# Kernel tuning notes

Hardware: AMD Instinct MI355X
Metric: run time of the kernel (lower is better)

Reference implementation:

```python
import jax, jax.numpy as jnp
import numpy as np
import math

B, NX, NY = 4, 64, 64
IN_DIM, OUT_DIM = 3, 3
DIM, DEPTH, HEADS, DH, FF_MULT = 192, 6, 8, 64, 4
INNER = HEADS * DH              # 512
FF = DIM * FF_MULT              # 768
M = int(DH * math.log(DH))      # 266 random features (performer default)
GROUPS = 8
LATENT_STEPS = 1
EPS_SN, EPS_K, EPS_GN = 1e-5, 1e-4, 1e-5


def setup_inputs() -> dict:
    rng = np.random.default_rng(0)
    f = lambda *s: jnp.asarray(rng.standard_normal(s).astype(np.float32) * 0.02)
    # unitary forward operator (SVD-whitened in torch == orthogonal matrix)
    Q, _ = np.linalg.qr(rng.standard_normal((DIM, DIM)).astype(np.float32))
    return {
        "x": jnp.asarray(rng.standard_normal((B, NX, NY, IN_DIM)).astype(np.float32)),
        "to_in_w": f(DIM, IN_DIM), "to_in_b": f(DIM),
        "pos_emb": f(1, NX * NY, DIM),
        "proj": jnp.asarray(rng.standard_normal((DEPTH, M, DH)).astype(np.float32)),
        "sn_attn_g": jnp.ones((DEPTH,), jnp.float32),
        "wq": f(DEPTH, INNER, DIM), "wk": f(DEPTH, INNER, DIM), "wv": f(DEPTH, INNER, DIM),
        "wo": f(DEPTH, DIM, INNER), "bo": f(DEPTH, DIM),
        "sn_ff_g": jnp.ones((DEPTH,), jnp.float32),
        "w1": f(DEPTH, FF, DIM), "b1": f(DEPTH, FF),
        "w2": f(DEPTH, DIM, FF), "b2": f(DEPTH, DIM),
        "expand_w": f(DIM, DIM),
        "fwd_w": jnp.asarray(Q.astype(np.float32)),
        "dec_lin_w": f(DIM, DIM), "dec_lin_b": f(DIM),
        "gn_g": jnp.ones((DIM,), jnp.float32), "gn_b": jnp.zeros((DIM,), jnp.float32),
        "c9_w": f(DIM, DIM // GROUPS, 9, 9), "c9_b": f(DIM),
        "c7_w": f(DIM // 2, DIM // GROUPS, 7, 7), "c7_b": f(DIM // 2),
        "c5_w": f(DIM // 4, (DIM // 2) // GROUPS, 5, 5), "c5_b": f(DIM // 4),
        "c1_w": f(OUT_DIM, DIM // 4, 1, 1), "c1_b": f(OUT_DIM),
        "latent_steps": LATENT_STEPS,
    }


def _scalenorm(x, g):
    n = jnp.linalg.norm(x, axis=-1, keepdims=True) * (x.shape[-1] ** -0.5)
    return x / jnp.maximum(n, EPS_SN) * g


def _softmax_features(data, proj, is_query):
    # data: [b,h,n,d]; proj: [m,d] -> FAVOR+ softmax-kernel features [b,h,n,m]
    dn = data.shape[-1] ** -0.25
    ratio = proj.shape[0] ** -0.5
    dd = jnp.einsum('bhnd,md->bhnm', data * dn, proj)
    diag = 0.5 * jnp.sum(data * data, -1) * (dn * dn)  # [b,h,n]
    if is_query:
        mx = jnp.max(dd, axis=-1, keepdims=True)
    else:
        mx = jnp.max(dd, axis=(-1, -2), keepdims=True)
    return ratio * (jnp.exp(dd - diag[..., None] - mx) + EPS_K)


def _attn(x, proj, wq, wk, wv, wo, bo):
    b, n, _ = x.shape
    split = lambda t: t.reshape(b, n, HEADS, DH).transpose(0, 2, 1, 3)
    q = split(x @ wq.T); k = split(x @ wk.T); v = split(x @ wv.T)
    qp = _softmax_features(q, proj, True)
    kp = _softmax_features(k, proj, False)
    context = jnp.einsum('bhnm,bhnd->bhmd', kp, v)            # [b,h,m,d]
    denom = jnp.einsum('bhnm,bhm->bhn', qp, kp.sum(2))
    out = jnp.einsum('bhnm,bhmd->bhnd', qp, context) / denom[..., None]
    out = out.transpose(0, 2, 1, 3).reshape(b, n, INNER)
    return out @ wo.T + bo


def _circ_conv(x, w, b, groups):
    p = w.shape[-1] // 2
    x = jnp.pad(x, ((0, 0), (0, 0), (p, p), (p, p)), mode='wrap')
    y = jax.lax.conv_general_dilated(x, w, (1, 1), 'VALID',
        dimension_numbers=('NCHW', 'OIHW', 'NCHW'), feature_group_count=groups)
    return y + b[None, :, None, None]


def _group_norm(x, g, b):
    B_, C, H, W = x.shape
    xg = x.reshape(B_, GROUPS, C // GROUPS, H, W)
    mu = xg.mean((2, 3, 4), keepdims=True)
    var = xg.var((2, 3, 4), keepdims=True)
    xn = ((xg - mu) * jax.lax.rsqrt(var + EPS_GN)).reshape(B_, C, H, W)
    return xn * g[None, :, None, None] + b[None, :, None, None]


def reference(x, to_in_w, to_in_b, pos_emb, proj, sn_attn_g, wq, wk, wv, wo, bo,
              sn_ff_g, w1, b1, w2, b2, expand_w, fwd_w, dec_lin_w, dec_lin_b,
              gn_g, gn_b, c9_w, c9_b, c7_w, c7_b, c5_w, c5_b, c1_w, c1_b, latent_steps):
    b, nx, ny, _ = x.shape
    h = x @ to_in_w.T + to_in_b                       # [b,nx,ny,dim]
    h = h.reshape(b, nx * ny, DIM) + pos_emb[:, :nx * ny]
    for i in range(DEPTH):                             # Performer: prenorm attn + prenorm FF
        h = h + _attn(_scalenorm(h, sn_attn_g[i]), proj[i], wq[i], wk[i], wv[i], wo[i], bo[i])
        hn = _scalenorm(h, sn_ff_g[i])
        h = h + (jax.nn.gelu(hn @ w1[i].T + b1[i], approximate=False) @ w2[i].T + b2[i])
    h = h.reshape(b, nx, ny, DIM) @ expand_w.T        # expand_latent (no bias)
    u, us = h, []
    for _ in range(latent_steps):
        u = u @ fwd_w.T                               # unitary forward operator
        us.append(u)
    u = jnp.concatenate(us, 0)                        # [(b*t), nx, ny, c]
    y = u @ dec_lin_w.T + dec_lin_b
    y = y.transpose(0, 3, 1, 2)                       # NCHW
    y = _group_norm(y, gn_g, gn_b)
    y = jax.nn.gelu(_circ_conv(y, c9_w, c9_b, GROUPS), approximate=False)
    y = jax.nn.gelu(_circ_conv(y, c7_w, c7_b, GROUPS), approximate=False)
    y = jax.nn.gelu(_circ_conv(y, c5_w, c5_b, GROUPS), approximate=False)
    y = jax.lax.conv_general_dilated(y, c1_w, (1, 1), 'VALID',
        dimension_numbers=('NCHW', 'OIHW', 'NCHW')) + c1_b[None, :, None, None]
    # einops '(b t) c nx ny -> b t nx ny c'
    y = y.reshape(b, latent_steps, OUT_DIM, nx, ny).transpose(0, 1, 3, 4, 2)
    return y
```

## Files before the change

kernel.cpp:

```cpp
#include <hip/hip_runtime.h>
#include <cmath>

#define NB      4
#define NTOK    4096
#define BNTOK   16384
#define CDIM    192
#define CINNER  512
#define NHEADS  8
#define DHEAD   64
#define CFF     768
#define MFEAT   266
#define NDEPTH  6

#define DN      0.35355339059327373f
#define RATIO   0.06131393394849658f

typedef unsigned short u16;
typedef __attribute__((ext_vector_type(8))) short s16x8;
typedef __attribute__((ext_vector_type(8))) u16  u16x8;
typedef __attribute__((ext_vector_type(4))) float f32x4;

#define OFF_H    0ull
#define OFF_HN   3145728ull
#define OFF_Q    6291456ull
#define OFF_K    14680064ull
#define OFF_V    23068672ull
#define OFF_BIG  31457280ull
#define OFF_PJ   44040192ull
#define OFF_CTXT 44163072ull
#define OFF_KMAX 47368192ull
#define OFF_GNP  47368448ull
#define OFF_GNS  47369472ull
#define OFF_WHI  47370240ull
#define OFF_WLO  49489920ull
#define WOFF_QKV 0ull
#define WOFF_WO  1769472ull
#define WOFF_W1  2359296ull
#define WOFF_W2  3244032ull
#define WOFF_EXP 4128768ull
#define WOFF_FWD 4165632ull
#define WOFF_DEC 4202496ull

#define PJL      20480
#define CTXTN    819200

__device__ __forceinline__ float gelu_f(float x) {
    return 0.5f * x * (1.0f + erff(x * 0.7071067811865476f));
}
__device__ __forceinline__ unsigned f2ord(float f) {
    int i = __float_as_int(f);
    return (i >= 0) ? ((unsigned)i | 0x80000000u) : (unsigned)(~i);
}
__device__ __forceinline__ float ord2f(unsigned u) {
    int i = (u & 0x80000000u) ? (int)(u & 0x7fffffffu) : ~(int)u;
    return __int_as_float(i);
}
__device__ __forceinline__ void split_bf16(float a, u16& h, u16& l) {
    unsigned ua = __float_as_uint(a);
    unsigned rh = (ua + 0x7FFFu + ((ua >> 16) & 1u)) >> 16;
    h = (u16)rh;
    float hf = __uint_as_float(rh << 16);
    float lo = a - hf;
    unsigned ul = __float_as_uint(lo);
    unsigned rl = (ul + 0x7FFFu + ((ul >> 16) & 1u)) >> 16;
    l = (u16)rl;
}
__device__ __forceinline__ u16 hi_bf16(float a) {
    unsigned ua = __float_as_uint(a);
    return (u16)((ua + 0x7FFFu + ((ua >> 16) & 1u)) >> 16);
}

__global__ __launch_bounds__(256) void cvt_qkv(const float* __restrict__ wq,
    const float* __restrict__ wk, const float* __restrict__ wv,
    u16* __restrict__ hi, u16* __restrict__ lo)
{
    int idx = blockIdx.x * 256 + threadIdx.x;
    int l = idx / 294912, rem = idx - l * 294912;
    int r = rem / 192, c = rem - r * 192;
    float v;
    if (r < 512)       v = wq[((size_t)l * 512 + r) * 192 + c];
    else if (r < 1024) v = wk[((size_t)l * 512 + (r - 512)) * 192 + c];
    else               v = wv[((size_t)l * 512 + (r - 1024)) * 192 + c];
    u16 h, lw; split_bf16(v, h, lw);
    hi[idx] = h; lo[idx] = lw;
}

__global__ __launch_bounds__(256) void cvt_w(const float* __restrict__ src,
    u16* __restrict__ hi, u16* __restrict__ lo, int n)
{
    int idx = blockIdx.x * 256 + threadIdx.x;
    if (idx < n) {
        u16 h, l; split_bf16(src[idx], h, l);
        hi[idx] = h; lo[idx] = l;
    }
}

__global__ __launch_bounds__(256) void cvt_dec(const float* __restrict__ e,
    const float* __restrict__ f, const float* __restrict__ d,
    u16* __restrict__ hi, u16* __restrict__ lo)
{
    int idx = blockIdx.x * 256 + threadIdx.x;
    if (idx >= 110592) return;
    int which = idx / 36864, rem = idx - which * 36864;
    float v = (which == 0) ? e[rem] : (which == 1) ? f[rem] : d[rem];
    u16 h, l; split_bf16(v, h, l);
    hi[idx] = h; lo[idx] = l;
}

__global__ __launch_bounds__(256) void cvt_pj(const float* __restrict__ proj,
    u16* __restrict__ hi, u16* __restrict__ lo)
{
    int idx = blockIdx.x * 256 + threadIdx.x;
    int l = idx / PJL, rem = idx - l * PJL;
    int m = rem >> 6, k = rem & 63;
    float v = (m < MFEAT) ? proj[(size_t)l * MFEAT * DHEAD + m * 64 + k] : 0.f;
    u16 h, lw; split_bf16(v, h, lw);
    hi[idx] = h; lo[idx] = lw;
}

__global__ __launch_bounds__(256) void input_embed(const float* __restrict__ x,
    const float* __restrict__ w, const float* __restrict__ bvec,
    const float* __restrict__ pos, float* __restrict__ h)
{
    int idx = blockIdx.x * 256 + threadIdx.x;
    int row = idx / CDIM, c = idx - row * CDIM;
    int p = row & (NTOK - 1);
    const float* xr = x + (size_t)row * 3;
    h[idx] = xr[0]*w[c*3+0] + xr[1]*w[c*3+1] + xr[2]*w[c*3+2] + bvec[c] + pos[(size_t)p*CDIM + c];
}

__global__ __launch_bounds__(256) void scalenorm_kernel(const float* __restrict__ in,
    float* __restrict__ out, const float* __restrict__ gptr, int gidx)
{
    int wv = threadIdx.x >> 6, lane = threadIdx.x & 63;
    int row = blockIdx.x * 4 + wv;
    const float* p = in + (size_t)row * CDIM;
    float x0 = p[lane], x1 = p[lane + 64], x2 = p[lane + 128];
    float ss = x0*x0 + x1*x1 + x2*x2;
    #pragma unroll
    for (int off = 32; off; off >>= 1) ss += __shfl_xor(ss, off);
    float g = gptr[gidx];
    float n = sqrtf(ss * (1.0f / 192.0f));
    float s = g / fmaxf(n, 1e-5f);
    float* o = out + (size_t)row * CDIM;
    o[lane] = x0 * s; o[lane + 64] = x1 * s; o[lane + 128] = x2 * s;
}

#define LP 40
__global__ __launch_bounds__(256) void gemm_mfma(const float* __restrict__ A,
    const u16* __restrict__ Bhi, const u16* __restrict__ Blo,
    const float* __restrict__ bias, const float* __restrict__ resid,
    float* __restrict__ C, int M, int N, int K, int epi)
{
    __shared__ u16 a_hi[128 * LP], a_lo[128 * LP], b_hi[128 * LP], b_lo[128 * LP];
    const int tid = threadIdx.x;
    const int n0 = blockIdx.x * 128, m0 = blockIdx.y * 128;
    const int wave = tid >> 6, lane = tid & 63;
    const int wr = wave >> 1, wc = wave & 1;
    const int fr = lane & 15, q = lane >> 4;
    const bool wactive = (n0 + wc * 64) < N;
    f32x4 acc[4][4];
    #pragma unroll
    for (int i = 0; i < 4; ++i)
        #pragma unroll
        for (int j = 0; j < 4; ++j) { acc[i][j][0]=0.f; acc[i][j][1]=0.f; acc[i][j][2]=0.f; acc[i][j][3]=0.f; }

    const int srow = tid >> 1, sc0 = (tid & 1) * 16;
    const float* aptr = A + (size_t)(m0 + srow) * K + sc0;
    const bool bval = (n0 + srow) < N;
    const u16* bhp = Bhi + (size_t)(n0 + srow) * K + sc0;
    const u16* blp = Blo + (size_t)(n0 + srow) * K + sc0;
    const int soff = srow * LP + sc0;
    const int aoffb = (wr * 64 + fr) * LP + q * 8;
    const int boffb = (wc * 64 + fr) * LP + q * 8;

    for (int kc = 0; kc < K; kc += 32) {
        float4 f0 = *(const float4*)(aptr + kc);
        float4 f1 = *(const float4*)(aptr + kc + 4);
        float4 f2 = *(const float4*)(aptr + kc + 8);
        float4 f3 = *(const float4*)(aptr + kc + 12);
        u16x8 h0, l0, h1, l1;
        {
            float v[16] = {f0.x,f0.y,f0.z,f0.w, f1.x,f1.y,f1.z,f1.w,
                           f2.x,f2.y,f2.z,f2.w, f3.x,f3.y,f3.z,f3.w};
            u16 hh[16], ll[16];
            #pragma unroll
            for (int i = 0; i < 16; ++i) split_bf16(v[i], hh[i], ll[i]);
            #pragma unroll
            for (int i = 0; i < 8; ++i) { h0[i]=hh[i]; l0[i]=ll[i]; h1[i]=hh[8+i]; l1[i]=ll[8+i]; }
        }
        *(u16x8*)&a_hi[soff]     = h0;  *(u16x8*)&a_hi[soff + 8] = h1;
        *(u16x8*)&a_lo[soff]     = l0;  *(u16x8*)&a_lo[soff + 8] = l1;
        u16x8 bh0 = (u16x8)0, bh1 = (u16x8)0, bl0 = (u16x8)0, bl1 = (u16x8)0;
        if (bval) {
            bh0 = *(const u16x8*)(bhp + kc);  bh1 = *(const u16x8*)(bhp + kc + 8);
            bl0 = *(const u16x8*)(blp + kc);  bl1 = *(const u16x8*)(blp + kc + 8);
        }
        *(u16x8*)&b_hi[soff]     = bh0;  *(u16x8*)&b_hi[soff + 8] = bh1;
        *(u16x8*)&b_lo[soff]     = bl0;  *(u16x8*)&b_lo[soff + 8] = bl1;
        __syncthreads();
        if (wactive) {
            s16x8 Ah[4], Al[4], Bh[4], Bl[4];
            #pragma unroll
            for (int t = 0; t < 4; ++t) {
                Ah[t] = *(const s16x8*)&a_hi[aoffb + t * 16 * LP];
                Al[t] = *(const s16x8*)&a_lo[aoffb + t * 16 * LP];
                Bh[t] = *(const s16x8*)&b_hi[boffb + t * 16 * LP];
                Bl[t] = *(const s16x8*)&b_lo[boffb + t * 16 * LP];
            }
            #pragma unroll
            for (int i = 0; i < 4; ++i)
                #pragma unroll
                for (int j = 0; j < 4; ++j)
                    acc[i][j] = __builtin_amdgcn_mfma_f32_16x16x32_bf16(Ah[i], Bh[j], acc[i][j], 0, 0, 0);
            #pragma unroll
            for (int i = 0; i < 4; ++i)
                #pragma unroll
                for (int j = 0; j < 4; ++j)
                    acc[i][j] = __builtin_amdgcn_mfma_f32_16x16x32_bf16(Ah[i], Bl[j], acc[i][j], 0, 0, 0);
            #pragma unroll
            for (int i = 0; i < 4; ++i)
                #pragma unroll
                for (int j = 0; j < 4; ++j)
                    acc[i][j] = __builtin_amdgcn_mfma_f32_16x16x32_bf16(Al[i], Bh[j], acc[i][j], 0, 0, 0);
        }
        __syncthreads();
    }
    const int c0 = n0 + wc * 64;
    const int rowb = m0 + wr * 64;
    #pragma unroll
    for (int j = 0; j < 4; ++j) {
        int c = c0 + j * 16 + fr;
        if (c >= N) continue;
        float bb = (epi & 1) ? bias[c] : 0.f;
        float* cp;
        if (epi & 8) cp = C + (size_t)(c >> 9) * 8388608ull + (size_t)(c & 511);
        else         cp = C + c;
        const float* rp = (epi & 4) ? (resid + c) : nullptr;
        #pragma unroll
        for (int i = 0; i < 4; ++i) {
            #pragma unroll
            for (int r = 0; r < 4; ++r) {
                int row = rowb + i * 16 + q * 4 + r;
                float val = acc[i][j][r] + bb;
                if (epi & 2) val = gelu_f(val);
                if (epi & 4) val += rp[(size_t)row * N];
                size_t off = (epi & 8) ? (size_t)row * 512 : (size_t)row * N;
                cp[off] = val;
            }
        }
    }
}

__global__ void kmax_init(unsigned* kmaxu) {
    if (threadIdx.x < NDEPTH * 32) kmaxu[threadIdx.x] = 0u;
}

__global__ __launch_bounds__(256) void kmax2_kernel(const float* __restrict__ Km,
    const u16* __restrict__ pjh, unsigned* __restrict__ kmaxu)
{
    __shared__ __align__(16) u16 khi[64 * 72];
    __shared__ float wred[4];
    const int tid = threadIdx.x;
    const int nt = blockIdx.x, bh = blockIdx.y;
    const int b = bh >> 3, hh = bh & 7;
    const int wave = tid >> 6, lane = tid & 63;
    const int fr = lane & 15, quad = lane >> 4;
    float lm = -1e30f;
    const size_t kbase = ((size_t)b * NTOK) * CINNER + hh * DHEAD;
    for (int ch = 0; ch < 4; ++ch) {
        const int n0 = nt * 256 + ch * 64;
        __syncthreads();
        {
            int tok = tid >> 2, koff = (tid & 3) * 16;
            const float* kp = Km + kbase + (size_t)(n0 + tok) * CINNER + koff;
            u16 hh16[16];
            #pragma unroll
            for (int qd = 0; qd < 4; ++qd) {
                float4 f = *(const float4*)(kp + qd * 4);
                hh16[qd*4+0] = hi_bf16(f.x * DN); hh16[qd*4+1] = hi_bf16(f.y * DN);
                hh16[qd*4+2] = hi_bf16(f.z * DN); hh16[qd*4+3] = hi_bf16(f.w * DN);
            }
            u16x8 v0, v1;
            #pragma unroll
            for (int i = 0; i < 8; ++i) { v0[i] = hh16[i]; v1[i] = hh16[8+i]; }
            *(u16x8*)&khi[tok * 72 + koff] = v0;
            *(u16x8*)&khi[tok * 72 + koff + 8] = v1;
        }
        __syncthreads();
        int rowA = (wave * 16 + fr) * 72;
        s16x8 A0 = *(const s16x8*)&khi[rowA + quad * 8];
        s16x8 A1 = *(const s16x8*)&khi[rowA + 32 + quad * 8];
        for (int ct = 0; ct < 17; ++ct) {
            const u16* bp = pjh + (ct * 16 + fr) * 64 + quad * 8;
            s16x8 B0 = *(const s16x8*)bp;
            s16x8 B1 = *(const s16x8*)(bp + 32);
            f32x4 t; t[0]=0.f; t[1]=0.f; t[2]=0.f; t[3]=0.f;
            t = __builtin_amdgcn_mfma_f32_16x16x32_bf16(A0, B0, t, 0, 0, 0);
            t = __builtin_amdgcn_mfma_f32_16x16x32_bf16(A1, B1, t, 0, 0, 0);
            if (ct * 16 + fr < MFEAT) {
                #pragma unroll
                for (int r = 0; r < 4; ++r) lm = fmaxf(lm, t[r]);
            }
        }
    }
    #pragma unroll
    for (int off = 32; off; off >>= 1) lm = fmaxf(lm, __shfl_xor(lm, off));
    if (lane == 0) wred[wave] = lm;
    __syncthreads();
    if (tid == 0) {
        float m = fmaxf(fmaxf(wred[0], wred[1]), fmaxf(wred[2], wred[3]));
        atomicMax(kmaxu + bh, f2ord(m));
    }
}

__global__ __launch_bounds__(256) void ctx2_kernel(const float* __restrict__ Km,
    const float* __restrict__ Vm, const u16* __restrict__ pjh, const u16* __restrict__ pjl,
    const unsigned* __restrict__ kmaxu, float* __restrict__ part)
{
    __shared__ __align__(16) u16 khi[32 * 72], klo[32 * 72];
    __shared__ __align__(16) u16 vth[80 * 40], vtl[80 * 40];
    __shared__ __align__(16) u16 kph[4][16 * 40], kpl[4][16 * 40];
    __shared__ float diag[32];
    const int tid = threadIdx.x;
    const int bh = blockIdx.x, seg = blockIdx.y;
    const int b = bh >> 3, hh = bh & 7;
    const int wave = tid >> 6, lane = tid & 63;
    const int fr = lane & 15, quad = lane >> 4;
    const float kmx = ord2f(kmaxu[bh]);
    for (int i = tid; i < 16 * 40; i += 256) {
        int row = 64 + i / 40, col = i - (i / 40) * 40;
        vth[row * 40 + col] = (row == 64) ? (u16)0x3F80 : (u16)0;
        vtl[row * 40 + col] = 0;
    }
    f32x4 accv[5][5];
    #pragma unroll
    for (int i = 0; i < 5; ++i)
        #pragma unroll
        for (int j = 0; j < 5; ++j) { accv[i][j][0]=0.f; accv[i][j][1]=0.f; accv[i][j][2]=0.f; accv[i][j][3]=0.f; }
    const size_t rowbase = ((size_t)b * NTOK) * CINNER + hh * DHEAD;
    u16* sh = kph[wave];  u16* sl = kpl[wave];
    for (int nc = 0; nc < 16; ++nc) {
        const int n0 = seg * 512 + nc * 32;
        __syncthreads();
        {
            int tok = tid >> 3, koff = (tid & 7) * 8;
            const float* kp = Km + rowbase + (size_t)(n0 + tok) * CINNER + koff;
            float4 f0 = *(const float4*)kp;
            float4 f1 = *(const float4*)(kp + 4);
            float v[8] = {f0.x*DN, f0.y*DN, f0.z*DN, f0.w*DN, f1.x*DN, f1.y*DN, f1.z*DN, f1.w*DN};
            u16x8 hv, lv; float ps = 0.f;
            #pragma unroll
            for (int i = 0; i < 8; ++i) { u16 h, l; split_bf16(v[i], h, l); hv[i]=h; lv[i]=l; ps += v[i]*v[i]; }
            *(u16x8*)&khi[tok * 72 + koff] = hv;
            *(u16x8*)&klo[tok * 72 + koff] = lv;
            ps += __shfl_xor(ps, 1); ps += __shfl_xor(ps, 2); ps += __shfl_xor(ps, 4);
            if ((tid & 7) == 0) diag[tok] = 0.5f * ps;
            const float* vp = Vm + rowbase + (size_t)(n0 + tok) * CINNER + koff;
            float4 g0 = *(const float4*)vp;
            float4 g1 = *(const float4*)(vp + 4);
            float vv[8] = {g0.x, g0.y, g0.z, g0.w, g1.x, g1.y, g1.z, g1.w};
            #pragma unroll
            for (int i = 0; i < 8; ++i) {
                u16 h, l; split_bf16(vv[i], h, l);
                vth[(koff + i) * 40 + tok] = h;
                vtl[(koff + i) * 40 + tok] = l;
            }
        }
        __syncthreads();
        s16x8 Ah[2][2], Al[2][2];
        #pragma unroll
        for (int rt = 0; rt < 2; ++rt) {
            int rowA = (rt * 16 + fr) * 72;
            Ah[rt][0] = *(const s16x8*)&khi[rowA + quad * 8];
            Ah[rt][1] = *(const s16x8*)&khi[rowA + 32 + quad * 8];
            Al[rt][0] = *(const s16x8*)&klo[rowA + quad * 8];
            Al[rt][1] = *(const s16x8*)&klo[rowA + 32 + quad * 8];
        }
        for (int mc = 0; mc < 5; ++mc) {
            const int ct = mc * 4 + wave;
            const u16* bph = pjh + (ct * 16 + fr) * 64 + quad * 8;
            const u16* bpl = pjl + (ct * 16 + fr) * 64 + quad * 8;
            s16x8 B0h = *(const s16x8*)bph, B1h = *(const s16x8*)(bph + 32);
            s16x8 B0l = *(const s16x8*)bpl, B1l = *(const s16x8*)(bpl + 32);
            const bool valid = (ct * 16 + fr) < MFEAT;
            #pragma unroll
            for (int rt = 0; rt < 2; ++rt) {
                f32x4 dd; dd[0]=0.f; dd[1]=0.f; dd[2]=0.f; dd[3]=0.f;
                dd = __builtin_amdgcn_mfma_f32_16x16x32_bf16(Ah[rt][0], B0h, dd, 0, 0, 0);
                dd = __builtin_amdgcn_mfma_f32_16x16x32_bf16(Ah[rt][0], B0l, dd, 0, 0, 0);
                dd = __builtin_amdgcn_mfma_f32_16x16x32_bf16(Al[rt][0], B0h, dd, 0, 0, 0);
                dd = __builtin_amdgcn_mfma_f32_16x16x32_bf16(Ah[rt][1], B1h, dd, 0, 0, 0);
                dd = __builtin_amdgcn_mfma_f32_16x16x32_bf16(Ah[rt][1], B1l, dd, 0, 0, 0);
                dd = __builtin_amdgcn_mfma_f32_16x16x32_bf16(Al[rt][1], B1h, dd, 0, 0, 0);
                ushort4 ph, pl;
                #pragma unroll
                for (int r = 0; r < 4; ++r) {
                    float dgv = diag[rt * 16 + quad * 4 + r];
                    float val = valid ? RATIO * (expf(dd[r] - dgv - kmx) + 1e-4f) : 0.f;
                    u16 h, l; split_bf16(val, h, l);
                    (&ph.x)[r] = h; (&pl.x)[r] = l;
                }
                *(ushort4*)&sh[fr * 40 + rt * 16 + quad * 4] = ph;
                *(ushort4*)&sl[fr * 40 + rt * 16 + quad * 4] = pl;
            }
            s16x8 Bh = *(const s16x8*)&sh[fr * 40 + quad * 8];
            s16x8 Bl = *(const s16x8*)&sl[fr * 40 + quad * 8];
            #pragma unroll
            for (int rt2 = 0; rt2 < 5; ++rt2) {
                s16x8 Vh = *(const s16x8*)&vth[(rt2 * 16 + fr) * 40 + quad * 8];
                s16x8 Vl = *(const s16x8*)&vtl[(rt2 * 16 + fr) * 40 + quad * 8];
                accv[rt2][mc] = __builtin_amdgcn_mfma_f32_16x16x32_bf16(Vh, Bh, accv[rt2][mc], 0, 0, 0);
                accv[rt2][mc] = __builtin_amdgcn_mfma_f32_16x16x32_bf16(Vh, Bl, accv[rt2][mc], 0, 0, 0);
                accv[rt2][mc] = __builtin_amdgcn_mfma_f32_16x16x32_bf16(Vl, Bh, accv[rt2][mc], 0, 0, 0);
            }
        }
    }
    float* pb = part + ((size_t)(seg * 32 + bh)) * 80 * 320;
    #pragma unroll
    for (int rt2 = 0; rt2 < 5; ++rt2) {
        #pragma unroll
        for (int mc = 0; mc < 5; ++mc) {
            int ct = mc * 4 + wave;
            #pragma unroll
            for (int r = 0; r < 4; ++r)
                pb[(size_t)(rt2 * 16 + quad * 4 + r) * 320 + ct * 16 + fr] = accv[rt2][mc][r];
        }
    }
}

__global__ __launch_bounds__(256) void ctxt_reduce(const float* __restrict__ part,
    u16* __restrict__ cth, u16* __restrict__ ctl)
{
    int idx = blockIdx.x * 256 + threadIdx.x;
    float s = 0.f;
    #pragma unroll
    for (int sg = 0; sg < 8; ++sg) s += part[(size_t)sg * CTXTN + idx];
    u16 h, l; split_bf16(s, h, l);
    cth[idx] = h; ctl[idx] = l;
}

__global__ __launch_bounds__(256) void qside2_kernel(const float* __restrict__ Qm,
    const u16* __restrict__ pjh, const u16* __restrict__ pjl,
    const u16* __restrict__ cth, const u16* __restrict__ ctl,
    float* __restrict__ attn_out)
{
    __shared__ __align__(16) u16 qhi[64 * 72], qlo[64 * 72];
    __shared__ __align__(16) u16 slabh[4][16 * 72], slabl[4][16 * 72];
    __shared__ float diag[64];
    const int tid = threadIdx.x;
    const int nt = blockIdx.x, bh = blockIdx.y;
    const int b = bh >> 3, hh = bh & 7;
    const int wave = tid >> 6, lane = tid & 63;
    const int fr = lane & 15, quad = lane >> 4;
    const int n0 = nt * 64;
    {
        int tok = tid >> 2, koff = (tid & 3) * 16;
        const float* qp = Qm + ((size_t)(b * NTOK + n0 + tok)) * CINNER + hh * DHEAD + koff;
        float v[16]; float ps = 0.f;
        #pragma unroll
        for (int qd = 0; qd < 4; ++qd) {
            float4 f = *(const float4*)(qp + qd * 4);
            v[qd*4+0]=f.x*DN; v[qd*4+1]=f.y*DN; v[qd*4+2]=f.z*DN; v[qd*4+3]=f.w*DN;
        }
        u16x8 h0, l0, h1, l1;
        #pragma unroll
        for (int i = 0; i < 8; ++i) {
            u16 h, l; split_bf16(v[i], h, l); h0[i]=h; l0[i]=l;
            split_bf16(v[8+i], h, l); h1[i]=h; l1[i]=l;
        }
        #pragma unroll
        for (int i = 0; i < 16; ++i) ps += v[i]*v[i];
        *(u16x8*)&qhi[tok * 72 + koff] = h0;  *(u16x8*)&qhi[tok * 72 + koff + 8] = h1;
        *(u16x8*)&qlo[tok * 72 + koff] = l0;  *(u16x8*)&qlo[tok * 72 + koff + 8] = l1;
        ps += __shfl_xor(ps, 1); ps += __shfl_xor(ps, 2);
        if ((tid & 3) == 0) diag[tok] = 0.5f * ps;
    }
    __syncthreads();
    f32x4 dd[20];
    #pragma unroll
    for (int ct = 0; ct < 20; ++ct) { dd[ct][0]=0.f; dd[ct][1]=0.f; dd[ct][2]=0.f; dd[ct][3]=0.f; }
    {
        int rowA = (wave * 16 + fr) * 72;
        s16x8 A0h = *(const s16x8*)&qhi[rowA + quad * 8];
        s16x8 A1h = *(const s16x8*)&qhi[rowA + 32 + quad * 8];
        s16x8 A0l = *(const s16x8*)&qlo[rowA + quad * 8];
        s16x8 A1l = *(const s16x8*)&qlo[rowA + 32 + quad * 8];
        #pragma unroll
        for (int ct = 0; ct < 20; ++ct) {
            const u16* bph = pjh + (ct * 16 + fr) * 64 + quad * 8;
            const u16* bpl = pjl + (ct * 16 + fr) * 64 + quad * 8;
            s16x8 B0h = *(const s16x8*)bph, B1h = *(const s16x8*)(bph + 32);
            s16x8 B0l = *(const s16x8*)bpl, B1l = *(const s16x8*)(bpl + 32);
            dd[ct] = __builtin_amdgcn_mfma_f32_16x16x32_bf16(A0h, B0h, dd[ct], 0, 0, 0);
            dd[ct] = __builtin_amdgcn_mfma_f32_16x16x32_bf16(A0h, B0l, dd[ct], 0, 0, 0);
            dd[ct] = __builtin_amdgcn_mfma_f32_16x16x32_bf16(A0l, B0h, dd[ct], 0, 0, 0);
            dd[ct] = __builtin_amdgcn_mfma_f32_16x16x32_bf16(A1h, B1h, dd[ct], 0, 0, 0);
            dd[ct] = __builtin_amdgcn_mfma_f32_16x16x32_bf16(A1h, B1l, dd[ct], 0, 0, 0);
            dd[ct] = __builtin_amdgcn_mfma_f32_16x16x32_bf16(A1l, B1h, dd[ct], 0, 0, 0);
        }
    }
    float pm[4] = {-1e30f, -1e30f, -1e30f, -1e30f};
    #pragma unroll
    for (int ct = 0; ct < 20; ++ct) {
        if (ct * 16 + fr < MFEAT) {
            #pragma unroll
            for (int r = 0; r < 4; ++r) pm[r] = fmaxf(pm[r], dd[ct][r]);
        }
    }
    #pragma unroll
    for (int r = 0; r < 4; ++r) {
        pm[r] = fmaxf(pm[r], __shfl_xor(pm[r], 1));
        pm[r] = fmaxf(pm[r], __shfl_xor(pm[r], 2));
        pm[r] = fmaxf(pm[r], __shfl_xor(pm[r], 4));
        pm[r] = fmaxf(pm[r], __shfl_xor(pm[r], 8));
    }
    float dg[4];
    #pragma unroll
    for (int r = 0; r < 4; ++r) dg[r] = diag[wave * 16 + quad * 4 + r];
    #pragma unroll
    for (int ct = 0; ct < 20; ++ct) {
        bool valid = (ct * 16 + fr) < MFEAT;
        #pragma unroll
        for (int r = 0; r < 4; ++r)
            dd[ct][r] = valid ? RATIO * (expf(dd[ct][r] - dg[r] - pm[r]) + 1e-4f) : 0.f;
    }
    f32x4 acc[5];
    #pragma unroll
    for (int dt = 0; dt < 5; ++dt) { acc[dt][0]=0.f; acc[dt][1]=0.f; acc[dt][2]=0.f; acc[dt][3]=0.f; }
    u16* sh = slabh[wave];  u16* sl = slabl[wave];
    for (int mc = 0; mc < 5; ++mc) {
        #pragma unroll
        for (int c = 0; c < 4; ++c) {
            int ct = mc * 4 + c;
            #pragma unroll
            for (int r = 0; r < 4; ++r) {
                u16 h, l; split_bf16(dd[ct][r], h, l);
                int tok = quad * 4 + r;
                sh[tok * 72 + c * 16 + fr] = h;
                sl[tok * 72 + c * 16 + fr] = l;
            }
        }
        #pragma unroll
        for (int ks = 0; ks < 2; ++ks) {
            s16x8 Ah = *(const s16x8*)&sh[fr * 72 + ks * 32 + quad * 8];
            s16x8 Al = *(const s16x8*)&sl[fr * 72 + ks * 32 + quad * 8];
            #pragma unroll
            for (int dt = 0; dt < 5; ++dt) {
                const u16* bph = cth + ((size_t)bh * 80 + dt * 16 + fr) * 320 + mc * 64 + ks * 32 + quad * 8;
                const u16* bpl = ctl + ((size_t)bh * 80 + dt * 16 + fr) * 320 + mc * 64 + ks * 32 + quad * 8;
                s16x8 Bh = *(const s16x8*)bph;
                s16x8 Bl = *(const s16x8*)bpl;
                acc[dt] = __builtin_amdgcn_mfma_f32_16x16x32_bf16(Ah, Bh, acc[dt], 0, 0, 0);
                acc[dt] = __builtin_amdgcn_mfma_f32_16x16x32_bf16(Ah, Bl, acc[dt], 0, 0, 0);
                acc[dt] = __builtin_amdgcn_mfma_f32_16x16x32_bf16(Al, Bh, acc[dt], 0, 0, 0);
            }
        }
    }
    #pragma unroll
    for (int r = 0; r < 4; ++r) {
        float denom = __shfl(acc[4][r], lane & 48);
        float inv = 1.0f / denom;
        int token = n0 + wave * 16 + quad * 4 + r;
        float* op = attn_out + ((size_t)(b * NTOK + token)) * CINNER + hh * DHEAD;
        #pragma unroll
        for (int dt = 0; dt < 4; ++dt)
            op[dt * 16 + fr] = acc[dt][r] * inv;
    }
}

__global__ __launch_bounds__(256) void gn_part_kernel(const float* __restrict__ y,
    float2* __restrict__ part)
{
    __shared__ float s_s[256], s_q[256];
    const int tid = threadIdx.x;
    const int sp = blockIdx.x, g = blockIdx.y, b = blockIdx.z;
    int p = sp * 256 + tid;
    const float* base = y + ((size_t)(b * NTOK + p)) * CDIM + g * 24;
    float s = 0.f, q = 0.f;
    #pragma unroll
    for (int i = 0; i < 24; ++i) { float v = base[i]; s += v; q += v * v; }
    s_s[tid] = s; s_q[tid] = q;
    __syncthreads();
    for (int st = 128; st; st >>= 1) {
        if (tid < st) { s_s[tid] += s_s[tid + st]; s_q[tid] += s_q[tid + st]; }
        __syncthreads();
    }
    if (tid == 0) part[(b * 8 + g) * 16 + sp] = make_float2(s_s[0], s_q[0]);
}

__global__ void gn_stat_kernel(const float2* __restrict__ part, float2* __restrict__ stat)
{
    int bg = threadIdx.x;
    if (bg < 32) {
        float s = 0.f, q = 0.f;
        for (int i = 0; i < 16; ++i) { float2 v = part[bg * 16 + i]; s += v.x; q += v.y; }
        float mean = s * (1.0f / 98304.0f);
        float var = q * (1.0f / 98304.0f) - mean * mean;
        stat[bg] = make_float2(mean, rsqrtf(var + 1e-5f));
    }
}

__global__ __launch_bounds__(256) void gn_apply_kernel(const float* __restrict__ y,
    const float2* __restrict__ stat, const float* __restrict__ gg,
    const float* __restrict__ gb, float* __restrict__ out)
{
    __shared__ float tile[64][65];
    const int tid = threadIdx.x;
    const int pt = blockIdx.x, ct = blockIdx.y, b = blockIdx.z;
    const int p0 = pt * 64, c0 = ct * 64;
    #pragma unroll
    for (int r = 0; r < 4; ++r) {
        int id = tid + r * 256;
        int pr = id >> 4, kq = (id & 15) * 4;
        float4 v = *(const float4*)(y + ((size_t)(b * NTOK + p0 + pr)) * CDIM + c0 + kq);
        tile[pr][kq+0] = v.x; tile[pr][kq+1] = v.y; tile[pr][kq+2] = v.z; tile[pr][kq+3] = v.w;
    }
    __syncthreads();
    const int cc = tid >> 6, pp = tid & 63;
    #pragma unroll
    for (int i = 0; i < 16; ++i) {
        int c = c0 + cc * 16 + i;
        int g = c / 24;
        float2 st = stat[b * 8 + g];
        float v = tile[pp][cc * 16 + i];
        out[((size_t)(b * CDIM + c)) * NTOK + p0 + pp] = (v - st.x) * st.y * gg[c] + gb[c];
    }
}

template<int KS, int CIN, int COUT, int OX, int YS, int OCB>
__global__ __launch_bounds__(256) void circ_conv2(const float* __restrict__ in,
    const float* __restrict__ w, const float* __restrict__ bias,
    float* __restrict__ out, int do_gelu)
{
    constexpr int P   = KS / 2;
    constexpr int ICG = CIN / 8;
    constexpr int OCG = COUT / 8;
    constexpr int TW  = 64 + 2 * P;
    constexpr int TR  = 64 / YS + 2 * P;
    constexpr int RS0 = (TW + 3) & ~3;
    constexpr int RS  = (RS0 % 8 == 0) ? RS0 + 4 : RS0;
    constexpr int TCX = 64 / OX;
    constexpr int RV  = (OX + KS - 1 + 3) & ~3;
    __shared__ __align__(16) float tile[TR * RS];
    const int tid = threadIdx.x;
    const int oc0 = blockIdx.x * OCB;
    const int y0  = blockIdx.y * (64 / YS);
    const int b   = blockIdx.z;
    const int g   = oc0 / OCG;
    const int tx  = tid % TCX, ty = tid / TCX;
    float acc[OCB][OX] = {};
    const float* ip0 = in + ((size_t)(b * CIN + g * ICG)) * 4096;
    #pragma unroll 1
    for (int ic = 0; ic < ICG; ++ic) {
        __syncthreads();
        const float* ip = ip0 + (size_t)ic * 4096;
        for (int idx = tid; idx < TR * TW; idx += 256) {
            int r = idx / TW, c = idx - r * TW;
            int gy = (y0 + r - P) & 63, gx = (c - P) & 63;
            tile[r * RS + c] = ip[gy * 64 + gx];
        }
        __syncthreads();
        const float* wp = w + ((size_t)oc0 * ICG + ic) * (KS * KS);
        #pragma unroll 1
        for (int ky = 0; ky < KS; ++ky) {
            float wreg[OCB][KS];
            #pragma unroll
            for (int oc = 0; oc < OCB; ++oc)
                #pragma unroll
                for (int kx = 0; kx < KS; ++kx)
                    wreg[oc][kx] = wp[(size_t)oc * ICG * KS * KS + ky * KS + kx];
            float rv[RV];
            const float* rp = &tile[(ty + ky) * RS + tx * OX];
            #pragma unroll
            for (int q2 = 0; q2 < RV / 4; ++q2)
                *(float4*)&rv[q2 * 4] = *(const float4*)(rp + q2 * 4);
            #pragma unroll
            for (int kx = 0; kx < KS; ++kx)
                #pragma unroll
                for (int oc = 0; oc < OCB; ++oc)
                    #pragma unroll
                    for (int ox = 0; ox < OX; ++ox)
                        acc[oc][ox] += rv[kx + ox] * wreg[oc][kx];
        }
    }
    const int y = y0 + ty, x = tx * OX;
    #pragma unroll
    for (int oc = 0; oc < OCB; ++oc) {
        float bv = bias[oc0 + oc];
        float vo[OX];
        #pragma unroll
        for (int ox = 0; ox < OX; ++ox) {
            float vv = acc[oc][ox] + bv;
            vo[ox] = do_gelu ? gelu_f(vv) : vv;
        }
        float* op = out + (((size_t)(b * COUT + oc0 + oc) * 64 + y)) * 64 + x;
        #pragma unroll
        for (int q2 = 0; q2 < OX / 4; ++q2)
            *(float4*)(op + q2 * 4) = *(float4*)&vo[q2 * 4];
    }
}

__global__ __launch_bounds__(256) void conv1_kernel(const float* __restrict__ in,
    const float* __restrict__ w, const float* __restrict__ bias, float* __restrict__ out)
{
    int idx = blockIdx.x * 256 + threadIdx.x;
    int b = idx >> 12, p = idx & 4095;
    float a0 = bias[0], a1 = bias[1], a2 = bias[2];
    const float* ip = in + (size_t)b * 48 * NTOK + p;
    #pragma unroll 8
    for (int ic = 0; ic < 48; ++ic) {
        float v = ip[(size_t)ic * NTOK];
        a0 += v * w[ic]; a1 += v * w[48 + ic]; a2 += v * w[96 + ic];
    }
    float* op = out + (size_t)idx * 3;
    op[0] = a0; op[1] = a1; op[2] = a2;
}

static inline void gemm_mf(hipStream_t s, const float* A, const u16* Bhi, const u16* Blo,
                           const float* bias, const float* resid, float* C,
                           int M, int N, int K, int epi)
{
    dim3 g((N + 127) / 128, M / 128);
    hipLaunchKernelGGL(gemm_mfma, g, dim3(256), 0, s, A, Bhi, Blo, bias, resid, C, M, N, K, epi);
}

extern "C" void kernel_launch(void* const* d_in, const int* in_sizes, int n_in,
                              void* d_out, int out_size, void* d_ws, size_t ws_size,
                              hipStream_t stream)
{
    (void)in_sizes; (void)n_in; (void)out_size; (void)ws_size;
    const float* x        = (const float*)d_in[0];
    const float* to_in_w  = (const float*)d_in[1];
    const float* to_in_b  = (const float*)d_in[2];
    const float* pos_emb  = (const float*)d_in[3];
    const float* proj     = (const float*)d_in[4];
    const float* sn_attn_g= (const float*)d_in[5];
    const float* wq       = (const float*)d_in[6];
    const float* wk       = (const float*)d_in[7];
    const float* wv       = (const float*)d_in[8];
    const float* wo       = (const float*)d_in[9];
    const float* bo       = (const float*)d_in[10];
    const float* sn_ff_g  = (const float*)d_in[11];
    const float* w1       = (const float*)d_in[12];
    const float* b1       = (const float*)d_in[13];
    const float* w2       = (const float*)d_in[14];
    const float* b2       = (const float*)d_in[15];
    const float* expand_w = (const float*)d_in[16];
    const float* fwd_w    = (const float*)d_in[17];
    const float* dec_lin_w= (const float*)d_in[18];
    const float* dec_lin_b= (const float*)d_in[19];
    const float* gn_g     = (const float*)d_in[20];
    const float* gn_b     = (const float*)d_in[21];
    const float* c9_w     = (const float*)d_in[22];
    const float* c9_b     = (const float*)d_in[23];
    const float* c7_w     = (const float*)d_in[24];
    const float* c7_b     = (const float*)d_in[25];
    const float* c5_w     = (const float*)d_in[26];
    const float* c5_b     = (const float*)d_in[27];
    const float* c1_w     = (const float*)d_in[28];
    const float* c1_b     = (const float*)d_in[29];
    float* out = (float*)d_out;

    float* ws = (float*)d_ws;
    float* h   = ws + OFF_H;
    float* hn  = ws + OFF_HN;
    float* q   = ws + OFF_Q;
    float* k   = ws + OFF_K;
    float* v   = ws + OFF_V;
    float* big = ws + OFF_BIG;
    u16* pjhi = (u16*)(ws + OFF_PJ);
    u16* pjlo = pjhi + 6 * PJL;
    u16* cthi = (u16*)(ws + OFF_CTXT);
    u16* ctlo = cthi + CTXTN;
    unsigned* kmaxu = (unsigned*)(ws + OFF_KMAX);
    float2* gnp = (float2*)(ws + OFF_GNP);
    float2* gns = (float2*)(ws + OFF_GNS);
    u16* whi = (u16*)(ws + OFF_WHI);
    u16* wlo = (u16*)(ws + OFF_WLO);

    hipLaunchKernelGGL(input_embed, dim3(BNTOK * CDIM / 256), dim3(256), 0, stream,
                       x, to_in_w, to_in_b, pos_emb, h);
    hipLaunchKernelGGL(kmax_init, dim3(1), dim3(256), 0, stream, kmaxu);
    hipLaunchKernelGGL(cvt_qkv, dim3(6912), dim3(256), 0, stream, wq, wk, wv,
                       whi + WOFF_QKV, wlo + WOFF_QKV);
    hipLaunchKernelGGL(cvt_w, dim3(2304), dim3(256), 0, stream, wo, whi + WOFF_WO, wlo + WOFF_WO, 589824);
    hipLaunchKernelGGL(cvt_w, dim3(3456), dim3(256), 0, stream, w1, whi + WOFF_W1, wlo + WOFF_W1, 884736);
    hipLaunchKernelGGL(cvt_w, dim3(3456), dim3(256), 0, stream, w2, whi + WOFF_W2, wlo + WOFF_W2, 884736);
    hipLaunchKernelGGL(cvt_dec, dim3(432), dim3(256), 0, stream, expand_w, fwd_w, dec_lin_w,
                       whi + WOFF_EXP, wlo + WOFF_EXP);
    hipLaunchKernelGGL(cvt_pj, dim3(480), dim3(256), 0, stream, proj, pjhi, pjlo);

    for (int l = 0; l < NDEPTH; ++l) {
        const float* bo_l = bo + (size_t)l * CDIM;
        const float* b1_l = b1 + (size_t)l * CFF;
        const float* b2_l = b2 + (size_t)l * CDIM;
        const u16* pjh_l = pjhi + (size_t)l * PJL;
        const u16* pjl_l = pjlo + (size_t)l * PJL;
        unsigned* kmax_l = kmaxu + l * 32;

        hipLaunchKernelGGL(scalenorm_kernel, dim3(BNTOK / 4), dim3(256), 0, stream, h, hn, sn_attn_g, l);
        gemm_mf(stream, hn, whi + WOFF_QKV + (size_t)l * 294912, wlo + WOFF_QKV + (size_t)l * 294912,
                nullptr, nullptr, q, BNTOK, 1536, CDIM, 8);
        hipLaunchKernelGGL(kmax2_kernel, dim3(16, 32), dim3(256), 0, stream, k, pjh_l, kmax_l);
        hipLaunchKernelGGL(ctx2_kernel, dim3(32, 8), dim3(256), 0, stream, k, v, pjh_l, pjl_l, kmax_l, big);
        hipLaunchKernelGGL(ctxt_reduce, dim3(CTXTN / 256), dim3(256), 0, stream, big, cthi, ctlo);
        hipLaunchKernelGGL(qside2_kernel, dim3(64, 32), dim3(256), 0, stream, q, pjh_l, pjl_l, cthi, ctlo, k);
        gemm_mf(stream, k, whi + WOFF_WO + (size_t)l * 98304, wlo + WOFF_WO + (size_t)l * 98304,
                bo_l, h, h, BNTOK, CDIM, CINNER, 1 | 4);

        hipLaunchKernelGGL(scalenorm_kernel, dim3(BNTOK / 4), dim3(256), 0, stream, h, hn, sn_ff_g, l);
        gemm_mf(stream, hn, whi + WOFF_W1 + (size_t)l * 147456, wlo + WOFF_W1 + (size_t)l * 147456,
                b1_l, nullptr, big, BNTOK, CFF, CDIM, 1 | 2);
        gemm_mf(stream, big, whi + WOFF_W2 + (size_t)l * 147456, wlo + WOFF_W2 + (size_t)l * 147456,
                b2_l, h, h, BNTOK, CDIM, CFF, 1 | 4);
    }

    gemm_mf(stream, h, whi + WOFF_EXP, wlo + WOFF_EXP, nullptr, nullptr, hn, BNTOK, CDIM, CDIM, 0);
    gemm_mf(stream, hn, whi + WOFF_FWD, wlo + WOFF_FWD, nullptr, nullptr, h, BNTOK, CDIM, CDIM, 0);
    gemm_mf(stream, h, whi + WOFF_DEC, wlo + WOFF_DEC, dec_lin_b, nullptr, hn, BNTOK, CDIM, CDIM, 1);

    float* y0 = big;
    float* y1 = big + 3145728;
    float* y2 = big + 6291456;
    float* y3 = big + 7864320;
    hipLaunchKernelGGL(gn_part_kernel, dim3(16, 8, 4), dim3(256), 0, stream, hn, gnp);
    hipLaunchKernelGGL(gn_stat_kernel, dim3(1), dim3(32), 0, stream, gnp, gns);
    hipLaunchKernelGGL(gn_apply_kernel, dim3(64, 3, 4), dim3(256), 0, stream, hn, gns, gn_g, gn_b, y0);

    hipLaunchKernelGGL((circ_conv2<9, 192, 192, 4, 4, 2>), dim3(96, 4, 4), dim3(256), 0, stream,
                       y0, c9_w, c9_b, y1, 1);
    hipLaunchKernelGGL((circ_conv2<7, 192, 96, 4, 4, 2>), dim3(48, 4, 4), dim3(256), 0, stream,
                       y1, c7_w, c7_b, y2, 1);
    hipLaunchKernelGGL((circ_conv2<5, 96, 48, 4, 4, 2>), dim3(24, 4, 4), dim3(256), 0, stream,
                       y2, c5_w, c5_b, y3, 1);
    hipLaunchKernelGGL(conv1_kernel, dim3(BNTOK / 256), dim3(256), 0, stream, y3, c1_w, c1_b, out);
}
```

Before: 3.634 ms.

## Fold scalenorm into GEMM A-load and retile circular convolutions

The scalenorm kernel now writes only a per-row scale, and the GEMM multiplies A rows by that scale while splitting them to bf16. This removes a full write and re-read of the normalized activation before the QKV and FF1 GEMMs. Separately, the circular-conv kernels precompute their tile gather indices once per thread. They are also relaunched with larger tiles (8 outputs per thread in x, 3 output channels per block) to raise weight and tile reuse, at the cost of more registers per thread.

```diff
diff --git a/kernel.cpp b/kernel.cpp
--- a/kernel.cpp
+++ b/kernel.cpp
@@ -129,8 +129,8 @@
     h[idx] = xr[0]*w[c*3+0] + xr[1]*w[c*3+1] + xr[2]*w[c*3+2] + bvec[c] + pos[(size_t)p*CDIM + c];
 }
 
-__global__ __launch_bounds__(256) void scalenorm_kernel(const float* __restrict__ in,
-    float* __restrict__ out, const float* __restrict__ gptr, int gidx)
+__global__ __launch_bounds__(256) void rownorm_kernel(const float* __restrict__ in,
+    float* __restrict__ sv, const float* __restrict__ gptr, int gidx)
 {
     int wv = threadIdx.x >> 6, lane = threadIdx.x & 63;
     int row = blockIdx.x * 4 + wv;
@@ -139,15 +139,16 @@
     float ss = x0*x0 + x1*x1 + x2*x2;
     #pragma unroll
     for (int off = 32; off; off >>= 1) ss += __shfl_xor(ss, off);
-    float g = gptr[gidx];
-    float n = sqrtf(ss * (1.0f / 192.0f));
-    float s = g / fmaxf(n, 1e-5f);
-    float* o = out + (size_t)row * CDIM;
-    o[lane] = x0 * s; o[lane + 64] = x1 * s; o[lane + 128] = x2 * s;
+    if (lane == 0) {
+        float g = gptr[gidx];
+        float n = sqrtf(ss * (1.0f / 192.0f));
+        sv[row] = g / fmaxf(n, 1e-5f);
+    }
 }
 
 #define LP 40
 __global__ __launch_bounds__(256) void gemm_mfma(const float* __restrict__ A,
+    const float* __restrict__ ascale,
     const u16* __restrict__ Bhi, const u16* __restrict__ Blo,
     const float* __restrict__ bias, const float* __restrict__ resid,
     float* __restrict__ C, int M, int N, int K, int epi)
@@ -167,6 +168,7 @@
 
     const int srow = tid >> 1, sc0 = (tid & 1) * 16;
     const float* aptr = A + (size_t)(m0 + srow) * K + sc0;
+    const float as = ascale ? ascale[m0 + srow] : 1.0f;
     const bool bval = (n0 + srow) < N;
     const u16* bhp = Bhi + (size_t)(n0 + srow) * K + sc0;
     const u16* blp = Blo + (size_t)(n0 + srow) * K + sc0;
@@ -185,7 +187,7 @@
                            f2.x,f2.y,f2.z,f2.w, f3.x,f3.y,f3.z,f3.w};
             u16 hh[16], ll[16];
             #pragma unroll
-            for (int i = 0; i < 16; ++i) split_bf16(v[i], hh[i], ll[i]);
+            for (int i = 0; i < 16; ++i) { float sv = v[i] * as; split_bf16(sv, hh[i], ll[i]); }
             #pragma unroll
             for (int i = 0; i < 8; ++i) { h0[i]=hh[i]; l0[i]=ll[i]; h1[i]=hh[8+i]; l1[i]=ll[8+i]; }
         }
@@ -629,7 +631,7 @@
 }
 
 template<int KS, int CIN, int COUT, int OX, int YS, int OCB>
-__global__ __launch_bounds__(256) void circ_conv2(const float* __restrict__ in,
+__global__ __launch_bounds__(256) void circ_conv3(const float* __restrict__ in,
     const float* __restrict__ w, const float* __restrict__ bias,
     float* __restrict__ out, int do_gelu)
 {
@@ -642,6 +644,7 @@
     constexpr int RS  = (RS0 % 8 == 0) ? RS0 + 4 : RS0;
     constexpr int TCX = 64 / OX;
     constexpr int RV  = (OX + KS - 1 + 3) & ~3;
+    constexpr int NLD = (TR * TW + 255) / 256;
     __shared__ __align__(16) float tile[TR * RS];
     const int tid = threadIdx.x;
     const int oc0 = blockIdx.x * OCB;
@@ -649,17 +652,26 @@
     const int b   = blockIdx.z;
     const int g   = oc0 / OCG;
     const int tx  = tid % TCX, ty = tid / TCX;
+    int srcs[NLD], dsts[NLD];
+    #pragma unroll
+    for (int j = 0; j < NLD; ++j) {
+        int idx = tid + j * 256;
+        if (idx < TR * TW) {
+            int r = idx / TW, c = idx - r * TW;
+            int gy = (y0 + r - P) & 63, gx = (c - P) & 63;
+            srcs[j] = gy * 64 + gx;
+            dsts[j] = r * RS + c;
+        } else { srcs[j] = 0; dsts[j] = -1; }
+    }
     float acc[OCB][OX] = {};
     const float* ip0 = in + ((size_t)(b * CIN + g * ICG)) * 4096;
     #pragma unroll 1
     for (int ic = 0; ic < ICG; ++ic) {
         __syncthreads();
         const float* ip = ip0 + (size_t)ic * 4096;
-        for (int idx = tid; idx < TR * TW; idx += 256) {
-            int r = idx / TW, c = idx - r * TW;
-            int gy = (y0 + r - P) & 63, gx = (c - P) & 63;
-            tile[r * RS + c] = ip[gy * 64 + gx];
-        }
+        #pragma unroll
+        for (int j = 0; j < NLD; ++j)
+            if (dsts[j] >= 0) tile[dsts[j]] = ip[srcs[j]];
         __syncthreads();
         const float* wp = w + ((size_t)oc0 * ICG + ic) * (KS * KS);
         #pragma unroll 1
@@ -717,12 +729,13 @@
     op[0] = a0; op[1] = a1; op[2] = a2;
 }
 
-static inline void gemm_mf(hipStream_t s, const float* A, const u16* Bhi, const u16* Blo,
+static inline void gemm_mf(hipStream_t s, const float* A, const float* ascale,
+                           const u16* Bhi, const u16* Blo,
                            const float* bias, const float* resid, float* C,
                            int M, int N, int K, int epi)
 {
     dim3 g((N + 127) / 128, M / 128);
-    hipLaunchKernelGGL(gemm_mfma, g, dim3(256), 0, s, A, Bhi, Blo, bias, resid, C, M, N, K, epi);
+    hipLaunchKernelGGL(gemm_mfma, g, dim3(256), 0, s, A, ascale, Bhi, Blo, bias, resid, C, M, N, K, epi);
 }
 
 extern "C" void kernel_launch(void* const* d_in, const int* in_sizes, int n_in,
@@ -765,6 +778,7 @@
     float* ws = (float*)d_ws;
     float* h   = ws + OFF_H;
     float* hn  = ws + OFF_HN;
+    float* sbuf = ws + OFF_HN;
     float* q   = ws + OFF_Q;
     float* k   = ws + OFF_K;
     float* v   = ws + OFF_V;
@@ -799,26 +813,26 @@
         const u16* pjl_l = pjlo + (size_t)l * PJL;
         unsigned* kmax_l = kmaxu + l * 32;
 
-        hipLaunchKernelGGL(scalenorm_kernel, dim3(BNTOK / 4), dim3(256), 0, stream, h, hn, sn_attn_g, l);
-        gemm_mf(stream, hn, whi + WOFF_QKV + (size_t)l * 294912, wlo + WOFF_QKV + (size_t)l * 294912,
+        hipLaunchKernelGGL(rownorm_kernel, dim3(BNTOK / 4), dim3(256), 0, stream, h, sbuf, sn_attn_g, l);
+        gemm_mf(stream, h, sbuf, whi + WOFF_QKV + (size_t)l * 294912, wlo + WOFF_QKV + (size_t)l * 294912,
                 nullptr, nullptr, q, BNTOK, 1536, CDIM, 8);
         hipLaunchKernelGGL(kmax2_kernel, dim3(16, 32), dim3(256), 0, stream, k, pjh_l, kmax_l);
         hipLaunchKernelGGL(ctx2_kernel, dim3(32, 8), dim3(256), 0, stream, k, v, pjh_l, pjl_l, kmax_l, big);
         hipLaunchKernelGGL(ctxt_reduce, dim3(CTXTN / 256), dim3(256), 0, stream, big, cthi, ctlo);
         hipLaunchKernelGGL(qside2_kernel, dim3(64, 32), dim3(256), 0, stream, q, pjh_l, pjl_l, cthi, ctlo, k);
-        gemm_mf(stream, k, whi + WOFF_WO + (size_t)l * 98304, wlo + WOFF_WO + (size_t)l * 98304,
+        gemm_mf(stream, k, nullptr, whi + WOFF_WO + (size_t)l * 98304, wlo + WOFF_WO + (size_t)l * 98304,
                 bo_l, h, h, BNTOK, CDIM, CINNER, 1 | 4);
 
-        hipLaunchKernelGGL(scalenorm_kernel, dim3(BNTOK / 4), dim3(256), 0, stream, h, hn, sn_ff_g, l);
-        gemm_mf(stream, hn, whi + WOFF_W1 + (size_t)l * 147456, wlo + WOFF_W1 + (size_t)l * 147456,
+        hipLaunchKernelGGL(rownorm_kernel, dim3(BNTOK / 4), dim3(256), 0, stream, h, sbuf, sn_ff_g, l);
+        gemm_mf(stream, h, sbuf, whi + WOFF_W1 + (size_t)l * 147456, wlo + WOFF_W1 + (size_t)l * 147456,
                 b1_l, nullptr, big, BNTOK, CFF, CDIM, 1 | 2);
-        gemm_mf(stream, big, whi + WOFF_W2 + (size_t)l * 147456, wlo + WOFF_W2 + (size_t)l * 147456,
+        gemm_mf(stream, big, nullptr, whi + WOFF_W2 + (size_t)l * 147456, wlo + WOFF_W2 + (size_t)l * 147456,
                 b2_l, h, h, BNTOK, CDIM, CFF, 1 | 4);
     }
 
-    gemm_mf(stream, h, whi + WOFF_EXP, wlo + WOFF_EXP, nullptr, nullptr, hn, BNTOK, CDIM, CDIM, 0);
-    gemm_mf(stream, hn, whi + WOFF_FWD, wlo + WOFF_FWD, nullptr, nullptr, h, BNTOK, CDIM, CDIM, 0);
-    gemm_mf(stream, h, whi + WOFF_DEC, wlo + WOFF_DEC, dec_lin_b, nullptr, hn, BNTOK, CDIM, CDIM, 1);
+    gemm_mf(stream, h, nullptr, whi + WOFF_EXP, wlo + WOFF_EXP, nullptr, nullptr, hn, BNTOK, CDIM, CDIM, 0);
+    gemm_mf(stream, hn, nullptr, whi + WOFF_FWD, wlo + WOFF_FWD, nullptr, nullptr, h, BNTOK, CDIM, CDIM, 0);
+    gemm_mf(stream, h, nullptr, whi + WOFF_DEC, wlo + WOFF_DEC, dec_lin_b, nullptr, hn, BNTOK, CDIM, CDIM, 1);
 
     float* y0 = big;
     float* y1 = big + 3145728;
@@ -828,11 +842,11 @@
     hipLaunchKernelGGL(gn_stat_kernel, dim3(1), dim3(32), 0, stream, gnp, gns);
     hipLaunchKernelGGL(gn_apply_kernel, dim3(64, 3, 4), dim3(256), 0, stream, hn, gns, gn_g, gn_b, y0);
 
-    hipLaunchKernelGGL((circ_conv2<9, 192, 192, 4, 4, 2>), dim3(96, 4, 4), dim3(256), 0, stream,
+    hipLaunchKernelGGL((circ_conv3<9, 192, 192, 8, 2, 3>), dim3(64, 2, 4), dim3(256), 0, stream,
                        y0, c9_w, c9_b, y1, 1);
-    hipLaunchKernelGGL((circ_conv2<7, 192, 96, 4, 4, 2>), dim3(48, 4, 4), dim3(256), 0, stream,
+    hipLaunchKernelGGL((circ_conv3<7, 192, 96, 8, 2, 3>), dim3(32, 2, 4), dim3(256), 0, stream,
                        y1, c7_w, c7_b, y2, 1);
-    hipLaunchKernelGGL((circ_conv2<5, 96, 48, 4, 4, 2>), dim3(24, 4, 4), dim3(256), 0, stream,
+    hipLaunchKernelGGL((circ_conv3<5, 96, 48, 4, 4, 3>), dim3(16, 4, 4), dim3(256), 0, stream,
                        y2, c5_w, c5_b, y3, 1);
     hipLaunchKernelGGL(conv1_kernel, dim3(BNTOK / 256), dim3(256), 0, stream, y3, c1_w, c1_b, out);
 }
```

After: 3.613 ms. About the same (-0.6%).
